# Kernel optimization log

Measured on AMD Instinct MI355X. Metric: run time of the kernel, lower is better.

The kernel has to match this reference:

```python
import jax, jax.numpy as jnp
import numpy as np

N_HEAD = 16

def setup_inputs() -> dict:
    key = jax.random.key(0)
    ks = jax.random.split(key, 8)
    B, Sq, Sk, D = 4, 1024, 2048, 1024
    s = 0.02  # GPT-2 init scale for weights
    return {
        "x": jax.random.normal(ks[0], (B, Sq, D), jnp.float32),
        "ctx": jax.random.normal(ks[1], (B, Sk, D), jnp.float32),
        "attention_mask": jnp.zeros((B, 1, 1, Sk), jnp.float32),
        "Wq": jax.random.normal(ks[2], (D, D), jnp.float32) * s,
        "bq": jnp.zeros((D,), jnp.float32),
        "Wkv": jax.random.normal(ks[3], (D, 2 * D), jnp.float32) * s,
        "bkv": jnp.zeros((2 * D,), jnp.float32),
        "Wp": jax.random.normal(ks[4], (D, D), jnp.float32) * s,
        "bp": jnp.zeros((D,), jnp.float32),
    }

def _split_heads(t):
    # [B, S, D] -> [B, H, S, dh]
    B, S, D = t.shape
    return t.reshape(B, S, N_HEAD, D // N_HEAD).transpose(0, 2, 1, 3)

def reference(x, ctx, attention_mask, Wq, bq, Wkv, bkv, Wp, bp):
    B, Sq, D = x.shape
    dh = D // N_HEAD
    q = _split_heads(x @ Wq + bq)                       # [B,H,Sq,dh]
    kv = ctx @ Wkv + bkv                                # [B,Sk,2D]
    k = _split_heads(kv[..., :D])                       # [B,H,Sk,dh]
    v = _split_heads(kv[..., D:])                       # [B,H,Sk,dh]
    w = jnp.einsum("bhqd,bhkd->bhqk", q, k) / jnp.sqrt(jnp.float32(dh))
    w = w + attention_mask
    w = jax.nn.softmax(w, axis=-1)                      # attn_pdrop=0 -> no dropout
    a = jnp.einsum("bhqk,bhkd->bhqd", w, v)             # [B,H,Sq,dh]
    a = a.transpose(0, 2, 1, 3).reshape(B, Sq, D)       # merge heads
    return a @ Wp + bp                                  # resid_pdrop=0
```

## Files before the change

### kernel.cpp

```cpp
#include <hip/hip_runtime.h>
#include <stdint.h>

#define H_B  4
#define H_SQ 1024
#define H_SK 2048
#define H_D  1024
#define H_NH 16
#define H_DH 64

typedef __bf16 bf16x8 __attribute__((ext_vector_type(8)));
typedef float  f32x4  __attribute__((ext_vector_type(4)));

__device__ __forceinline__ uint16_t f2bf(float f) {
    union { float f; uint32_t u; } v; v.f = f;
    uint32_t r = v.u + 0x7fffu + ((v.u >> 16) & 1u);
    return (uint16_t)(r >> 16);
}

__device__ __forceinline__ void gload_lds16(const void* g, void* l) {
    __builtin_amdgcn_global_load_lds(
        (const __attribute__((address_space(1))) uint32_t*)g,
        (__attribute__((address_space(3))) uint32_t*)l, 16, 0, 0);
}

#define MFMA_BF16(a, b, c) __builtin_amdgcn_mfma_f32_16x16x32_bf16((a), (b), (c), 0, 0, 0)
#define EXP2(x) __builtin_amdgcn_exp2f(x)

template <int CTRL>
__device__ __forceinline__ float dpp_xor(float v) {
    return __builtin_bit_cast(float,
        __builtin_amdgcn_update_dpp(__builtin_bit_cast(int, v),
                                    __builtin_bit_cast(int, v),
                                    CTRL, 0xF, 0xF, false));
}
#define DPP_XOR1 0xB1
#define DPP_XOR2 0x4E
#define DPP_XOR4 0x141
#define DPP_XOR8 0x140

__device__ __forceinline__ float dpp_max16(float v) {
    v = fmaxf(v, dpp_xor<DPP_XOR1>(v));
    v = fmaxf(v, dpp_xor<DPP_XOR2>(v));
    v = fmaxf(v, dpp_xor<DPP_XOR4>(v));
    v = fmaxf(v, dpp_xor<DPP_XOR8>(v));
    return v;
}
__device__ __forceinline__ float dpp_sum16(float v) {
    v += dpp_xor<DPP_XOR1>(v);
    v += dpp_xor<DPP_XOR2>(v);
    v += dpp_xor<DPP_XOR4>(v);
    v += dpp_xor<DPP_XOR8>(v);
    return v;
}

__global__ void cvt2_bf16_kernel(const float* __restrict__ a, uint16_t* __restrict__ oa, int n4a,
                                 const float* __restrict__ b, uint16_t* __restrict__ ob, int n4b) {
    int i = blockIdx.x * blockDim.x + threadIdx.x;
    int stride = gridDim.x * blockDim.x;
    int tot = n4a + n4b;
    for (; i < tot; i += stride) {
        float4 v;
        if (i < n4a) v = ((const float4*)a)[i];
        else         v = ((const float4*)b)[i - n4a];
        ushort4 o;
        o.x = f2bf(v.x); o.y = f2bf(v.y); o.z = f2bf(v.z); o.w = f2bf(v.w);
        if (i < n4a) ((ushort4*)oa)[i] = o;
        else         ((ushort4*)ob)[i - n4a] = o;
    }
}

__global__ void wtrans3_kernel(const float* __restrict__ Wq, uint16_t* __restrict__ WqT,
                               const float* __restrict__ Wkv, uint16_t* __restrict__ WkvT,
                               const float* __restrict__ Wp, uint16_t* __restrict__ WpT) {
    __shared__ float tile[32][33];
    int bx = blockIdx.x;
    const float* W; uint16_t* WT; int N, n0;
    if (bx < 32)      { W = Wq;  WT = WqT;  N = 1024; n0 = bx * 32; }
    else if (bx < 96) { W = Wkv; WT = WkvT; N = 2048; n0 = (bx - 32) * 32; }
    else              { W = Wp;  WT = WpT;  N = 1024; n0 = (bx - 96) * 32; }
    int k0 = blockIdx.y * 32;
    int tx = threadIdx.x, ty = threadIdx.y;
    #pragma unroll
    for (int i = ty; i < 32; i += 8)
        tile[i][tx] = W[(size_t)(k0 + i) * N + n0 + tx];
    __syncthreads();
    #pragma unroll
    for (int i = ty; i < 32; i += 8)
        WT[(size_t)(n0 + i) * 1024 + k0 + tx] = f2bf(tile[tx][i]);
}

template <int MODE, int BM>
__global__ __launch_bounds__(256) void gemm_bt_kernel(
    const uint16_t* __restrict__ A, const uint16_t* __restrict__ BT,
    const float* __restrict__ bias, void* __restrict__ Cv,
    uint16_t* __restrict__ vTb, int M, int N, int K)
{
    constexpr int MI = BM / 32;
    __shared__ uint16_t As[2][BM * 32];
    __shared__ uint16_t Bs[2][128 * 32];

    int nbn = N >> 7;
    int nwg = gridDim.x;
    int cpx = nwg >> 3;
    int wg = blockIdx.x;
    wg = (wg & 7) * cpx + (wg >> 3);
    int bm = wg / nbn, bn = wg % nbn;

    int t = threadIdx.x;
    int w = t >> 6, l = t & 63;
    int lr = l & 15, lg = l >> 4;
    int wr = (w >> 1) * (BM / 2), wc = (w & 1) * 64;

    const uint16_t* Ab = A + (size_t)bm * BM * K;
    const uint16_t* Bb = BT + (size_t)bn * 128 * K;

    int ca = w * 64 + l;
    int rowa = ca >> 2, kpa = (ca & 3) * 8;
    int cb = 256 + ca;
    int rowb = cb >> 2, kpb = (cb & 3) * 8;
    int offa = ca * 16;
    int offb = cb * 16;

    f32x4 acc[MI][4];
    #pragma unroll
    for (int i = 0; i < MI; ++i)
        #pragma unroll
        for (int j = 0; j < 4; ++j) acc[i][j] = {0.f, 0.f, 0.f, 0.f};

    gload_lds16(Ab + (size_t)rowa * K + kpa, (char*)As[0] + (offa & ~1023));
    if constexpr (BM == 128)
        gload_lds16(Ab + (size_t)rowb * K + kpb, (char*)As[0] + (offb & ~1023));
    gload_lds16(Bb + (size_t)rowa * K + kpa, (char*)Bs[0] + (offa & ~1023));
    gload_lds16(Bb + (size_t)rowb * K + kpb, (char*)Bs[0] + (offb & ~1023));
    __syncthreads();

    int buf = 0;
    for (int k0 = 0; k0 < K; k0 += 32) {
        if (k0 + 32 < K) {
            int kn = k0 + 32;
            gload_lds16(Ab + (size_t)rowa * K + kn + kpa, (char*)As[buf ^ 1] + (offa & ~1023));
            if constexpr (BM == 128)
                gload_lds16(Ab + (size_t)rowb * K + kn + kpb, (char*)As[buf ^ 1] + (offb & ~1023));
            gload_lds16(Bb + (size_t)rowa * K + kn + kpa, (char*)Bs[buf ^ 1] + (offa & ~1023));
            gload_lds16(Bb + (size_t)rowb * K + kn + kpb, (char*)Bs[buf ^ 1] + (offb & ~1023));
        }
        bf16x8 af[MI], bf[4];
        #pragma unroll
        for (int mi = 0; mi < MI; ++mi)
            af[mi] = *(const bf16x8*)&As[buf][(wr + mi * 16 + lr) * 32 + lg * 8];
        #pragma unroll
        for (int ni = 0; ni < 4; ++ni)
            bf[ni] = *(const bf16x8*)&Bs[buf][(wc + ni * 16 + lr) * 32 + lg * 8];
        #pragma unroll
        for (int mi = 0; mi < MI; ++mi)
            #pragma unroll
            for (int ni = 0; ni < 4; ++ni)
                acc[mi][ni] = MFMA_BF16(af[mi], bf[ni], acc[mi][ni]);
        __syncthreads();
        buf ^= 1;
    }

    #pragma unroll
    for (int mi = 0; mi < MI; ++mi) {
        #pragma unroll
        for (int ni = 0; ni < 4; ++ni) {
            int col = bn * 128 + wc + ni * 16 + lr;
            float bv = bias[col];
            int row0 = bm * BM + wr + mi * 16 + lg * 4;
            if constexpr (MODE == 2) {
                if (col < H_D) {
                    uint16_t* kb = (uint16_t*)Cv;
                    #pragma unroll
                    for (int j = 0; j < 4; ++j)
                        kb[(size_t)(row0 + j) * H_D + col] = f2bf(acc[mi][ni][j] + bv);
                } else {
                    int dall = col - H_D;
                    int hh = dall >> 6, dd = dall & 63;
                    int bb = row0 >> 11, sk0 = row0 & 2047;
                    uint16_t p0 = f2bf(acc[mi][ni][0] + bv);
                    uint16_t p1 = f2bf(acc[mi][ni][1] + bv);
                    uint16_t p2 = f2bf(acc[mi][ni][2] + bv);
                    uint16_t p3 = f2bf(acc[mi][ni][3] + bv);
                    uint32_t lo = (uint32_t)p0 | ((uint32_t)p1 << 16);
                    uint32_t hi = (uint32_t)p2 | ((uint32_t)p3 << 16);
                    *(uint2*)&vTb[((size_t)(bb * 16 + hh) * 64 + dd) * H_SK + sk0] =
                        make_uint2(lo, hi);
                }
            } else {
                #pragma unroll
                for (int j = 0; j < 4; ++j) {
                    float v = acc[mi][ni][j] + bv;
                    if constexpr (MODE == 0)
                        ((uint16_t*)Cv)[(size_t)(row0 + j) * N + col] = f2bf(v);
                    else
                        ((float*)Cv)[(size_t)(row0 + j) * N + col] = v;
                }
            }
        }
    }
}

__global__ __launch_bounds__(256) void attn_kernel(
    const uint16_t* __restrict__ qb, const uint16_t* __restrict__ kb,
    const uint16_t* __restrict__ vT, const float* __restrict__ mask,
    uint16_t* __restrict__ ab)
{
    __shared__ uint16_t Ks[2][64 * 64];
    __shared__ uint16_t Vs[2][64 * 64];
    __shared__ uint16_t p_lds[4][16][64];

    int bid = blockIdx.x;
    int xcd = bid & 7;
    int kk = bid >> 3;
    int qt = kk & 15;
    int bh = xcd + 8 * (kk >> 4);
    int b = bh >> 4, hh = bh & 15;

    int t = threadIdx.x;
    int w = t >> 6, l = t & 63;
    int lr = l & 15, lg = l >> 4;

    const uint16_t* qrow = qb + (size_t)(b * H_SQ + qt * 64 + w * 16 + lr) * H_D + hh * H_DH;
    bf16x8 qf0 = *(const bf16x8*)(qrow + lg * 8);
    bf16x8 qf1 = *(const bf16x8*)(qrow + 32 + lg * 8);

    f32x4 acc[4];
    #pragma unroll
    for (int i = 0; i < 4; ++i) acc[i] = {0.f, 0.f, 0.f, 0.f};
    float mrow[4], lsum[4];
    #pragma unroll
    for (int j = 0; j < 4; ++j) { mrow[j] = -1e30f; lsum[j] = 0.f; }

    const float SC  = 0.18033688011112042f;
    const float L2E = 1.4426950408889634f;

    int c0 = w * 64 + l;
    int r0 = c0 >> 3,          gc0 = ((c0 & 7) ^ (r0 & 7)) * 8;
    int c1 = 256 + c0;
    int r1 = c1 >> 3,          gc1 = ((c1 & 7) ^ (r1 & 7)) * 8;
    int ldsoff = (w * 64) * 16;
    const uint16_t* kbase = kb + (size_t)b * H_SK * H_D + hh * H_DH;
    const uint16_t* vbase = vT + (size_t)bh * H_DH * H_SK;

    int xkbase = (lg & 1) << 5;
    int rdkey  = (lr & 7) << 3;

    float msk_nxt[4];
    {
        gload_lds16(kbase + (size_t)r0 * H_D + gc0, (char*)Ks[0] + ldsoff);
        gload_lds16(kbase + (size_t)r1 * H_D + gc1, (char*)Ks[0] + ldsoff + 4096);
        gload_lds16(vbase + (size_t)r0 * H_SK + gc0, (char*)Vs[0] + ldsoff);
        gload_lds16(vbase + (size_t)r1 * H_SK + gc1, (char*)Vs[0] + ldsoff + 4096);
        #pragma unroll
        for (int ni = 0; ni < 4; ++ni) msk_nxt[ni] = mask[b * H_SK + ni * 16 + lr] * L2E;
    }
    __syncthreads();

    int cur = 0;
    for (int kt = 0; kt < H_SK / 64; ++kt) {
        float msk_cur[4];
        #pragma unroll
        for (int ni = 0; ni < 4; ++ni) msk_cur[ni] = msk_nxt[ni];

        if (kt + 1 < H_SK / 64) {
            int sk1 = (kt + 1) * 64;
            int nxt = cur ^ 1;
            gload_lds16(kbase + (size_t)(sk1 + r0) * H_D + gc0, (char*)Ks[nxt] + ldsoff);
            gload_lds16(kbase + (size_t)(sk1 + r1) * H_D + gc1, (char*)Ks[nxt] + ldsoff + 4096);
            gload_lds16(vbase + (size_t)r0 * H_SK + sk1 + gc0, (char*)Vs[nxt] + ldsoff);
            gload_lds16(vbase + (size_t)r1 * H_SK + sk1 + gc1, (char*)Vs[nxt] + ldsoff + 4096);
            #pragma unroll
            for (int ni = 0; ni < 4; ++ni) msk_nxt[ni] = mask[b * H_SK + sk1 + ni * 16 + lr] * L2E;
        }

        const uint16_t* Kb = Ks[cur];
        const uint16_t* Vb = Vs[cur];
        int sw = (lg ^ (lr & 7)) * 8;

        f32x4 s[4];
        #pragma unroll
        for (int ni = 0; ni < 4; ++ni) s[ni] = {0.f, 0.f, 0.f, 0.f};
        #pragma unroll
        for (int ni = 0; ni < 4; ++ni) {
            bf16x8 kf0 = *(const bf16x8*)&Kb[(ni * 16 + lr) * 64 + sw];
            bf16x8 kf1 = *(const bf16x8*)&Kb[(ni * 16 + lr) * 64 + (sw ^ 32)];
            s[ni] = MFMA_BF16(qf0, kf0, s[ni]);
            s[ni] = MFMA_BF16(qf1, kf1, s[ni]);
        }

        float lg2[4][4], mx[4];
        #pragma unroll
        for (int j = 0; j < 4; ++j) {
            float a0 = fmaf(s[0][j], SC, msk_cur[0]);
            float a1 = fmaf(s[1][j], SC, msk_cur[1]);
            float a2 = fmaf(s[2][j], SC, msk_cur[2]);
            float a3 = fmaf(s[3][j], SC, msk_cur[3]);
            lg2[0][j] = a0; lg2[1][j] = a1; lg2[2][j] = a2; lg2[3][j] = a3;
            mx[j] = dpp_max16(fmaxf(fmaxf(a0, a1), fmaxf(a2, a3)));
        }
        int grow = 0;
        float nm[4];
        #pragma unroll
        for (int j = 0; j < 4; ++j) {
            nm[j] = fmaxf(mrow[j], mx[j]);
            grow |= (mx[j] > mrow[j] + 8.0f) ? 1 : 0;
        }
        if (__any(grow)) {
            #pragma unroll
            for (int j = 0; j < 4; ++j) {
                float alpha = EXP2(mrow[j] - nm[j]);
                mrow[j] = nm[j];
                lsum[j] *= alpha;
                #pragma unroll
                for (int ni = 0; ni < 4; ++ni) acc[ni][j] *= alpha;
            }
        }
        #pragma unroll
        for (int ni = 0; ni < 4; ++ni)
            #pragma unroll
            for (int j = 0; j < 4; ++j) {
                float p = EXP2(lg2[ni][j] - mrow[j]);
                lsum[j] += p;
                uint32_t pk;
                asm("v_cvt_pk_bf16_f32 %0, %1, %2" : "=v"(pk) : "v"(p), "v"(p));
                p_lds[w][lg * 4 + j][(ni * 16 + lr) ^ (xkbase | (j << 3))] = (uint16_t)pk;
            }

        int pc0 = (lg * 8) ^ rdkey;
        bf16x8 pf0 = *(const bf16x8*)&p_lds[w][lr][pc0];
        bf16x8 pf1 = *(const bf16x8*)&p_lds[w][lr][pc0 ^ 32];
        #pragma unroll
        for (int ni = 0; ni < 4; ++ni) {
            bf16x8 vf0 = *(const bf16x8*)&Vb[(ni * 16 + lr) * 64 + sw];
            bf16x8 vf1 = *(const bf16x8*)&Vb[(ni * 16 + lr) * 64 + (sw ^ 32)];
            acc[ni] = MFMA_BF16(pf0, vf0, acc[ni]);
            acc[ni] = MFMA_BF16(pf1, vf1, acc[ni]);
        }

        __syncthreads();
        cur ^= 1;
    }

    float inv[4];
    #pragma unroll
    for (int j = 0; j < 4; ++j) inv[j] = 1.0f / dpp_sum16(lsum[j]);
    #pragma unroll
    for (int ni = 0; ni < 4; ++ni)
        #pragma unroll
        for (int j = 0; j < 4; ++j) {
            int row = qt * 64 + w * 16 + lg * 4 + j;
            int col = hh * H_DH + ni * 16 + lr;
            ab[(size_t)(b * H_SQ + row) * H_D + col] = f2bf(acc[ni][j] * inv[j]);
        }
}

extern "C" void kernel_launch(void* const* d_in, const int* in_sizes, int n_in,
                              void* d_out, int out_size, void* d_ws, size_t ws_size,
                              hipStream_t stream) {
    const float* x    = (const float*)d_in[0];
    const float* ctx  = (const float*)d_in[1];
    const float* mask = (const float*)d_in[2];
    const float* Wq   = (const float*)d_in[3];
    const float* bq   = (const float*)d_in[4];
    const float* Wkv  = (const float*)d_in[5];
    const float* bkv  = (const float*)d_in[6];
    const float* Wp   = (const float*)d_in[7];
    const float* bp   = (const float*)d_in[8];
    float* out = (float*)d_out;

    char* ws = (char*)d_ws;
    uint16_t* xb   = (uint16_t*)(ws + 0);
    uint16_t* ctxb = (uint16_t*)(ws + 8388608);
    uint16_t* vTb  = (uint16_t*)(ws + 25165824);
    uint16_t* WqT  = (uint16_t*)(ws + 41943040);
    uint16_t* WkvT = (uint16_t*)(ws + 44040192);
    uint16_t* WpT  = (uint16_t*)(ws + 48234496);
    uint16_t* qb   = (uint16_t*)(ws + 50331648);
    uint16_t* kb   = (uint16_t*)(ws + 58720256);
    uint16_t* ab   = xb;

    cvt2_bf16_kernel<<<2048, 256, 0, stream>>>(x, xb, (H_B * H_SQ * H_D) / 4,
                                               ctx, ctxb, (H_B * H_SK * H_D) / 4);

    wtrans3_kernel<<<dim3(128, 32), dim3(32, 8), 0, stream>>>(Wq, WqT, Wkv, WkvT, Wp, WpT);

    gemm_bt_kernel<0, 64><<<512, 256, 0, stream>>>(xb,   WqT,  bq,  qb, nullptr, H_B * H_SQ, H_D,     H_D);
    gemm_bt_kernel<2, 128><<<1024, 256, 0, stream>>>(ctxb, WkvT, bkv, kb, vTb,   H_B * H_SK, 2 * H_D, H_D);

    attn_kernel<<<H_B * H_NH * (H_SQ / 64), 256, 0, stream>>>(qb, kb, vTb, mask, ab);

    gemm_bt_kernel<1, 64><<<512, 256, 0, stream>>>(ab, WpT, bp, out, nullptr, H_B * H_SQ, H_D, H_D);
}
```

Baseline: 197.5 us.

## Merge prep kernels and QKV GEMMs into single launches; defer row-max reduction

Folds the fp32-to-bf16 conversion and the weight transposes into one prep kernel, and folds the Q and KV projections into one GEMM launch that dispatches on block index into a shared GEMM body. The aim is fewer kernel launches, less tail idling between small kernels, and letting the Q and KV GEMMs fill the GPU together. In attention, the cross-lane max reduction moves inside the rare rescale branch, using the per-lane max for the threshold test. That removes DPP work from the common path. The cost is that the qkv kernel reserves 32KB of shared memory for every block, which can lower occupancy for the smaller Q tiles.

```diff
diff --git a/kernel.cpp b/kernel.cpp
--- a/kernel.cpp
+++ b/kernel.cpp
@@ -53,56 +53,61 @@
     return v;
 }
 
-__global__ void cvt2_bf16_kernel(const float* __restrict__ a, uint16_t* __restrict__ oa, int n4a,
-                                 const float* __restrict__ b, uint16_t* __restrict__ ob, int n4b) {
-    int i = blockIdx.x * blockDim.x + threadIdx.x;
-    int stride = gridDim.x * blockDim.x;
-    int tot = n4a + n4b;
-    for (; i < tot; i += stride) {
-        float4 v;
-        if (i < n4a) v = ((const float4*)a)[i];
-        else         v = ((const float4*)b)[i - n4a];
-        ushort4 o;
-        o.x = f2bf(v.x); o.y = f2bf(v.y); o.z = f2bf(v.z); o.w = f2bf(v.w);
-        if (i < n4a) ((ushort4*)oa)[i] = o;
-        else         ((ushort4*)ob)[i - n4a] = o;
+__global__ __launch_bounds__(256) void prep_kernel(
+    const float* __restrict__ x, uint16_t* __restrict__ xb,
+    const float* __restrict__ ctx, uint16_t* __restrict__ ctxb,
+    const float* __restrict__ Wq, uint16_t* __restrict__ WqT,
+    const float* __restrict__ Wkv, uint16_t* __restrict__ WkvT,
+    const float* __restrict__ Wp, uint16_t* __restrict__ WpT)
+{
+    __shared__ float tile[32][33];
+    int bid = blockIdx.x;
+    int t = threadIdx.x;
+    if (bid < 4096) {
+        int bx = bid & 127, k0 = (bid >> 7) * 32;
+        const float* W; uint16_t* WT; int N, n0;
+        if (bx < 32)      { W = Wq;  WT = WqT;  N = 1024; n0 = bx * 32; }
+        else if (bx < 96) { W = Wkv; WT = WkvT; N = 2048; n0 = (bx - 32) * 32; }
+        else              { W = Wp;  WT = WpT;  N = 1024; n0 = (bx - 96) * 32; }
+        int tx = t & 31, ty = t >> 5;
+        #pragma unroll
+        for (int i = ty; i < 32; i += 8)
+            tile[i][tx] = W[(size_t)(k0 + i) * N + n0 + tx];
+        __syncthreads();
+        #pragma unroll
+        for (int i = ty; i < 32; i += 8)
+            WT[(size_t)(n0 + i) * 1024 + k0 + tx] = f2bf(tile[tx][i]);
+    } else {
+        const int n4a = (H_B * H_SQ * H_D) / 4;
+        const int n4b = (H_B * H_SK * H_D) / 4;
+        int i = (bid - 4096) * 256 + t;
+        int stride = (gridDim.x - 4096) * 256;
+        int tot = n4a + n4b;
+        for (; i < tot; i += stride) {
+            float4 v;
+            if (i < n4a) v = ((const float4*)x)[i];
+            else         v = ((const float4*)ctx)[i - n4a];
+            ushort4 o;
+            o.x = f2bf(v.x); o.y = f2bf(v.y); o.z = f2bf(v.z); o.w = f2bf(v.w);
+            if (i < n4a) ((ushort4*)xb)[i] = o;
+            else         ((ushort4*)ctxb)[i - n4a] = o;
+        }
     }
 }
 
-__global__ void wtrans3_kernel(const float* __restrict__ Wq, uint16_t* __restrict__ WqT,
-                               const float* __restrict__ Wkv, uint16_t* __restrict__ WkvT,
-                               const float* __restrict__ Wp, uint16_t* __restrict__ WpT) {
-    __shared__ float tile[32][33];
-    int bx = blockIdx.x;
-    const float* W; uint16_t* WT; int N, n0;
-    if (bx < 32)      { W = Wq;  WT = WqT;  N = 1024; n0 = bx * 32; }
-    else if (bx < 96) { W = Wkv; WT = WkvT; N = 2048; n0 = (bx - 32) * 32; }
-    else              { W = Wp;  WT = WpT;  N = 1024; n0 = (bx - 96) * 32; }
-    int k0 = blockIdx.y * 32;
-    int tx = threadIdx.x, ty = threadIdx.y;
-    #pragma unroll
-    for (int i = ty; i < 32; i += 8)
-        tile[i][tx] = W[(size_t)(k0 + i) * N + n0 + tx];
-    __syncthreads();
-    #pragma unroll
-    for (int i = ty; i < 32; i += 8)
-        WT[(size_t)(n0 + i) * 1024 + k0 + tx] = f2bf(tile[tx][i]);
-}
-
 template <int MODE, int BM>
-__global__ __launch_bounds__(256) void gemm_bt_kernel(
+__device__ __forceinline__ void gemm_body(
     const uint16_t* __restrict__ A, const uint16_t* __restrict__ BT,
     const float* __restrict__ bias, void* __restrict__ Cv,
-    uint16_t* __restrict__ vTb, int M, int N, int K)
+    uint16_t* __restrict__ vTb, int M, int N, int K,
+    int wg, int nwg, char* smem)
 {
     constexpr int MI = BM / 32;
-    __shared__ uint16_t As[2][BM * 32];
-    __shared__ uint16_t Bs[2][128 * 32];
+    uint16_t (*As)[BM * 32] = (uint16_t (*)[BM * 32])smem;
+    uint16_t (*Bs)[128 * 32] = (uint16_t (*)[128 * 32])(smem + 2 * BM * 32 * 2);
 
     int nbn = N >> 7;
-    int nwg = gridDim.x;
     int cpx = nwg >> 3;
-    int wg = blockIdx.x;
     wg = (wg & 7) * cpx + (wg >> 3);
     int bm = wg / nbn, bn = wg % nbn;
 
@@ -200,6 +205,32 @@
     }
 }
 
+__global__ __launch_bounds__(256) void qkv_gemm_kernel(
+    const uint16_t* __restrict__ xb, const uint16_t* __restrict__ WqT,
+    const float* __restrict__ bq, uint16_t* __restrict__ qb,
+    const uint16_t* __restrict__ ctxb, const uint16_t* __restrict__ WkvT,
+    const float* __restrict__ bkv, uint16_t* __restrict__ kb,
+    uint16_t* __restrict__ vTb)
+{
+    __shared__ char smem[32768];
+    int bid = blockIdx.x;
+    if (bid < 512)
+        gemm_body<0, 64>(xb, WqT, bq, qb, nullptr, H_B * H_SQ, H_D, H_D,
+                         bid, 512, smem);
+    else
+        gemm_body<2, 128>(ctxb, WkvT, bkv, kb, vTb, H_B * H_SK, 2 * H_D, H_D,
+                          bid - 512, 1024, smem);
+}
+
+__global__ __launch_bounds__(256) void proj_gemm_kernel(
+    const uint16_t* __restrict__ ab, const uint16_t* __restrict__ WpT,
+    const float* __restrict__ bp, float* __restrict__ out)
+{
+    __shared__ char smem[24576];
+    gemm_body<1, 64>(ab, WpT, bp, out, nullptr, H_B * H_SQ, H_D, H_D,
+                     blockIdx.x, 512, smem);
+}
+
 __global__ __launch_bounds__(256) void attn_kernel(
     const uint16_t* __restrict__ qb, const uint16_t* __restrict__ kb,
     const uint16_t* __restrict__ vT, const float* __restrict__ mask,
@@ -288,7 +319,7 @@
             s[ni] = MFMA_BF16(qf1, kf1, s[ni]);
         }
 
-        float lg2[4][4], mx[4];
+        float lg2[4][4], mxl[4];
         #pragma unroll
         for (int j = 0; j < 4; ++j) {
             float a0 = fmaf(s[0][j], SC, msk_cur[0]);
@@ -296,20 +327,19 @@
             float a2 = fmaf(s[2][j], SC, msk_cur[2]);
             float a3 = fmaf(s[3][j], SC, msk_cur[3]);
             lg2[0][j] = a0; lg2[1][j] = a1; lg2[2][j] = a2; lg2[3][j] = a3;
-            mx[j] = dpp_max16(fmaxf(fmaxf(a0, a1), fmaxf(a2, a3)));
+            mxl[j] = fmaxf(fmaxf(a0, a1), fmaxf(a2, a3));
         }
         int grow = 0;
-        float nm[4];
-        #pragma unroll
-        for (int j = 0; j < 4; ++j) {
-            nm[j] = fmaxf(mrow[j], mx[j]);
-            grow |= (mx[j] > mrow[j] + 8.0f) ? 1 : 0;
-        }
+        #pragma unroll
+        for (int j = 0; j < 4; ++j)
+            grow |= (mxl[j] > mrow[j] + 8.0f) ? 1 : 0;
         if (__any(grow)) {
             #pragma unroll
             for (int j = 0; j < 4; ++j) {
-                float alpha = EXP2(mrow[j] - nm[j]);
-                mrow[j] = nm[j];
+                float mx = dpp_max16(mxl[j]);
+                float nm = fmaxf(mrow[j], mx);
+                float alpha = EXP2(mrow[j] - nm);
+                mrow[j] = nm;
                 lsum[j] *= alpha;
                 #pragma unroll
                 for (int ni = 0; ni < 4; ++ni) acc[ni][j] *= alpha;
@@ -379,15 +409,11 @@
     uint16_t* kb   = (uint16_t*)(ws + 58720256);
     uint16_t* ab   = xb;
 
-    cvt2_bf16_kernel<<<2048, 256, 0, stream>>>(x, xb, (H_B * H_SQ * H_D) / 4,
-                                               ctx, ctxb, (H_B * H_SK * H_D) / 4);
-
-    wtrans3_kernel<<<dim3(128, 32), dim3(32, 8), 0, stream>>>(Wq, WqT, Wkv, WkvT, Wp, WpT);
-
-    gemm_bt_kernel<0, 64><<<512, 256, 0, stream>>>(xb,   WqT,  bq,  qb, nullptr, H_B * H_SQ, H_D,     H_D);
-    gemm_bt_kernel<2, 128><<<1024, 256, 0, stream>>>(ctxb, WkvT, bkv, kb, vTb,   H_B * H_SK, 2 * H_D, H_D);
+    prep_kernel<<<7168, 256, 0, stream>>>(x, xb, ctx, ctxb, Wq, WqT, Wkv, WkvT, Wp, WpT);
+
+    qkv_gemm_kernel<<<1536, 256, 0, stream>>>(xb, WqT, bq, qb, ctxb, WkvT, bkv, kb, vTb);
 
     attn_kernel<<<H_B * H_NH * (H_SQ / 64), 256, 0, stream>>>(qb, kb, vTb, mask, ab);
 
-    gemm_bt_kernel<1, 64><<<512, 256, 0, stream>>>(ab, WpT, bp, out, nullptr, H_B * H_SQ, H_D, H_D);
-}
+    proj_gemm_kernel<<<512, 256, 0, stream>>>(ab, WpT, bp, out);
+}
```

After: 168.8 us. -14.5%, faster.
